# Performance work log

Hardware: AMD Instinct MI355X
Metric: run time of the kernel (lower is better)

## Reference

```python
import jax, jax.numpy as jnp
import numpy as np

# norse LIFCell defaults
DT = 1e-3
TAU_SYN_INV = 200.0   # 1 / 5e-3
TAU_MEM_INV = 100.0   # 1 / 1e-2
V_TH = 1.0
V_LEAK = 0.0
V_RESET = 0.0
ALPHA = 100.0         # superspike surrogate slope
BN_EPS = 1e-5

@jax.custom_vjp
def heaviside(x):
    return (x > 0).astype(x.dtype)

def _h_fwd(x):
    return (x > 0).astype(x.dtype), x

def _h_bwd(x, g):
    # superspike surrogate: d/dx H(x) ~ 1 / (alpha*|x| + 1)^2
    return (g / (ALPHA * jnp.abs(x) + 1.0) ** 2,)

heaviside.defvjp(_h_fwd, _h_bwd)

def _bn(x, g, b, m, v):
    # inference-mode BatchNorm1d with running stats
    return (x - m) * jax.lax.rsqrt(v + BN_EPS) * g + b

def _lif(inp, st):
    v, i = st
    v_dec = v + DT * TAU_MEM_INV * ((V_LEAK - v) + i)
    i_dec = i - DT * TAU_SYN_INV * i
    z = heaviside(v_dec - V_TH)
    v_new = (1.0 - z) * v_dec + z * V_RESET
    return z, (v_new, i_dec + inp)

B, F, T = 4096, 256, 100
H1, H2, H3, OUT = 128, 64, 32, 2

def setup_inputs():
    key = jax.random.key(0)
    ks = jax.random.split(key, 16)
    def lin(k, o, i):
        return jax.random.normal(k, (o, i), jnp.float32) / np.float32(np.sqrt(i))
    def bnp(k, n):
        k1, k2, k3, k4 = jax.random.split(k, 4)
        return (jax.random.normal(k1, (n,), jnp.float32) * 0.1 + 1.0,
                jax.random.normal(k2, (n,), jnp.float32) * 0.1,
                jax.random.normal(k3, (n,), jnp.float32) * 0.1,
                jax.random.uniform(k4, (n,), jnp.float32) + 0.5)
    bn0 = bnp(ks[0], F); bn1 = bnp(ks[1], H1); bn2 = bnp(ks[2], H2); bn3 = bnp(ks[3], H3)
    return {
        "spike_input": (jax.random.uniform(ks[4], (B, F, T)) < 0.2).astype(jnp.float32),
        "bn0_g": bn0[0], "bn0_b": bn0[1], "bn0_m": bn0[2], "bn0_v": bn0[3],
        "W1": lin(ks[5], H1, F), "b1": jnp.zeros((H1,), jnp.float32),
        "bn1_g": bn1[0], "bn1_b": bn1[1], "bn1_m": bn1[2], "bn1_v": bn1[3],
        "W2": lin(ks[6], H2, H1), "b2": jnp.zeros((H2,), jnp.float32),
        "bn2_g": bn2[0], "bn2_b": bn2[1], "bn2_m": bn2[2], "bn2_v": bn2[3],
        "W3": lin(ks[7], H3, H2), "b3": jnp.zeros((H3,), jnp.float32),
        "bn3_g": bn3[0], "bn3_b": bn3[1], "bn3_m": bn3[2], "bn3_v": bn3[3],
        "Wout": lin(ks[8], OUT, H3), "bout": jnp.zeros((OUT,), jnp.float32),
    }

def reference(spike_input, bn0_g, bn0_b, bn0_m, bn0_v,
              W1, b1, bn1_g, bn1_b, bn1_m, bn1_v,
              W2, b2, bn2_g, bn2_b, bn2_m, bn2_v,
              W3, b3, bn3_g, bn3_b, bn3_m, bn3_v,
              Wout, bout):
    bsz = spike_input.shape[0]
    dt = spike_input.dtype
    xt = jnp.transpose(spike_input, (2, 0, 1))  # [T, B, F]
    def zs(n):
        return (jnp.zeros((bsz, n), dt), jnp.zeros((bsz, n), dt))
    init = (zs(W1.shape[0]), zs(W2.shape[0]), zs(W3.shape[0]), zs(Wout.shape[0]),
            jnp.zeros((bsz, Wout.shape[0]), dt))
    def step(carry, x):
        st1, st2, st3, sto, acc = carry
        x = _bn(x, bn0_g, bn0_b, bn0_m, bn0_v)
        s1, st1 = _lif(_bn(x @ W1.T + b1, bn1_g, bn1_b, bn1_m, bn1_v), st1)
        s2, st2 = _lif(_bn(s1 @ W2.T + b2, bn2_g, bn2_b, bn2_m, bn2_v), st2)
        s3, st3 = _lif(_bn(s2 @ W3.T + b3, bn3_g, bn3_b, bn3_m, bn3_v), st3)
        so, sto = _lif(s3 @ Wout.T + bout, sto)
        return (st1, st2, st3, sto, acc + so), None
    carry, _ = jax.lax.scan(step, init, xt)
    return carry[4]  # [B, output_size] accumulated output spikes
```

## Files before the change

kernel.cpp:

```cpp
#include <hip/hip_runtime.h>
#include <stdint.h>

typedef unsigned int   uint32;
typedef unsigned short ushortT;
typedef short bf16x8 __attribute__((ext_vector_type(8)));
typedef float f32x4  __attribute__((ext_vector_type(4)));

#define T_REAL 100

#define W1S 0
#define W2S 98304
#define W3S 122880
#define WOS 129024
#define B1F 65280
#define B2F 65408
#define B3F 65472
#define BOF 65504

#define UB_BASE 33792
#define MK_BASE 68608
#define LDS_BYTES 81408

#define MFMA(a,b,c) __builtin_amdgcn_mfma_f32_16x16x32_bf16(a,b,c,0,0,0)

__device__ __forceinline__ ushortT bf16rne(float x) {
    uint32 u = __float_as_uint(x);
    return (ushortT)((u + 0x7FFFu + ((u >> 16) & 1u)) >> 16);
}

__device__ __forceinline__ void split3(float w, ushortT& a, ushortT& b, ushortT& c) {
    a = bf16rne(w); float fa = __uint_as_float((uint32)a << 16);
    float r1 = w - fa;
    b = bf16rne(r1); float fb = __uint_as_float((uint32)b << 16);
    float r2 = r1 - fb;
    c = bf16rne(r2);
}

__global__ void prep_w(const float* __restrict__ W1, const float* __restrict__ W2,
                       const float* __restrict__ W3, const float* __restrict__ Wo,
                       const float* __restrict__ bn0g, const float* __restrict__ bn0v,
                       const float* __restrict__ bn1g, const float* __restrict__ bn1v,
                       const float* __restrict__ bn2g, const float* __restrict__ bn2v,
                       const float* __restrict__ bn3g, const float* __restrict__ bn3v,
                       ushortT* __restrict__ wsS)
{
    int idx = blockIdx.x * 256 + threadIdx.x;
    float w; int base, size, off;
    if (idx < 32768) {
        int h = idx >> 8, f = idx & 255;
        float A = bn0g[f] / sqrtf(bn0v[f] + 1e-5f);
        float G = bn1g[h] / sqrtf(bn1v[h] + 1e-5f);
        w = W1[idx] * A * G; base = W1S; size = 32768; off = idx;
    } else if (idx < 40960) {
        int r = idx - 32768; int h = r >> 7;
        float G = bn2g[h] / sqrtf(bn2v[h] + 1e-5f);
        w = W2[r] * G; base = W2S; size = 8192; off = r;
    } else if (idx < 43008) {
        int r = idx - 40960; int h = r >> 6;
        float G = bn3g[h] / sqrtf(bn3v[h] + 1e-5f);
        w = W3[r] * G; base = W3S; size = 2048; off = r;
    } else if (idx < 43520) {
        int r = idx - 43008; int o = r >> 5, k = r & 31;
        w = (o < 2) ? Wo[o * 32 + k] : 0.f;
        base = WOS; size = 512; off = r;
    } else return;
    ushortT a, b, c; split3(w, a, b, c);
    wsS[base + off] = a; wsS[base + size + off] = b; wsS[base + 2 * size + off] = c;
}

__global__ void prep_bias(const float* __restrict__ bn0g, const float* __restrict__ bn0b,
                          const float* __restrict__ bn0m, const float* __restrict__ bn0v,
                          const float* __restrict__ b1,   const float* __restrict__ W1,
                          const float* __restrict__ bn1g, const float* __restrict__ bn1b,
                          const float* __restrict__ bn1m, const float* __restrict__ bn1v,
                          const float* __restrict__ b2,   const float* __restrict__ bn2g,
                          const float* __restrict__ bn2b, const float* __restrict__ bn2m,
                          const float* __restrict__ bn2v,
                          const float* __restrict__ b3,   const float* __restrict__ bn3g,
                          const float* __restrict__ bn3b, const float* __restrict__ bn3m,
                          const float* __restrict__ bn3v,
                          const float* __restrict__ bo,   float* __restrict__ wsF)
{
    __shared__ float Cs[256];
    const int tid = threadIdx.x;
    {
        float A = bn0g[tid] / sqrtf(bn0v[tid] + 1e-5f);
        Cs[tid] = bn0b[tid] - bn0m[tid] * A;
    }
    __syncthreads();
    if (tid < 128) {
        float G  = bn1g[tid] / sqrtf(bn1v[tid] + 1e-5f);
        float Bn = bn1b[tid] - bn1m[tid] * G;
        float s  = b1[tid];
        const float* wr = W1 + tid * 256;
        for (int f = 0; f < 256; ++f) s = fmaf(wr[f], Cs[f], s);
        wsF[B1F + tid] = G * s + Bn;
    }
    if (tid < 64) {
        float G = bn2g[tid] / sqrtf(bn2v[tid] + 1e-5f);
        wsF[B2F + tid] = G * b2[tid] + (bn2b[tid] - bn2m[tid] * G);
    }
    if (tid < 32) {
        float G = bn3g[tid] / sqrtf(bn3v[tid] + 1e-5f);
        wsF[B3F + tid] = G * b3[tid] + (bn3b[tid] - bn3m[tid] * G);
    }
    if (tid < 2) wsF[BOF + tid] = bo[tid];
}

__global__ __launch_bounds__(256, 2) void snn_main(
    const float* __restrict__ xin,
    const ushortT* __restrict__ wsS,
    const float* __restrict__ wsF,
    float* __restrict__ out)
{
    __shared__ uint4 ldsq[LDS_BYTES / 16];
    char* lds = (char*)ldsq;
    char* xw = lds;
    char* s1 = lds;
    char* s2 = lds;
    char* s3 = lds;
    float* u1 = (float*)(lds + UB_BASE);
    float* u2 = u1;
    float* u3 = u1;
    float* uo = u1;
    uint32* mk = (uint32*)(lds + MK_BASE);

    const int tid  = threadIdx.x;
    const int lane = tid & 63;
    const int wv   = tid >> 6;
    const int wvu  = __builtin_amdgcn_readfirstlane(wv);
    const int lr   = lane & 15;
    const int lg   = lane >> 4;
    const int b0   = blockIdx.x * 4;

    {
        const int fg = wvu;
        for (int s = 0; s < 4; ++s) {
            const float* rp = xin + ((size_t)(b0 + s) * 256 + fg * 64 + lane) * T_REAL;
            uint32* mrow = mk + (size_t)(s * 100) * 8 + fg * 2 + (lane >> 5);
#pragma unroll 1
            for (int q = 0; q < 25; ++q) {
                float4 v = *(const float4*)(rp + q * 4);
                unsigned long long bx = __ballot(v.x > 0.5f);
                unsigned long long by = __ballot(v.y > 0.5f);
                unsigned long long bz = __ballot(v.z > 0.5f);
                unsigned long long bw = __ballot(v.w > 0.5f);
                if ((lane & 31) == 0) {
                    const int sh = (lane >> 5) * 32;
                    mrow[(q * 4 + 0) * 8] = (uint32)(bx >> sh);
                    mrow[(q * 4 + 1) * 8] = (uint32)(by >> sh);
                    mrow[(q * 4 + 2) * 8] = (uint32)(bz >> sh);
                    mrow[(q * 4 + 3) * 8] = (uint32)(bw >> sh);
                }
            }
        }
    }

    float v1a = 0, i1a = 0, v1b = 0, i1b = 0;
    float v2a = 0, i2a = 0, v2b = 0, i2b = 0;
    float v3a = 0, i3a = 0, v3b = 0, i3b = 0;
    float vo = 0, io = 0, aspk = 0;

#pragma unroll 1
    for (int w = 0; w < 7; ++w) {
        const int t0 = w * 16;
        __syncthreads();

#pragma unroll
        for (int j = 0; j < 8; ++j) {
            const int c = tid + 256 * j;
            const int r = c >> 5, g = c & 31;
            const int s = r >> 4, tt = t0 + (r & 15);
            const int ttc = (tt < T_REAL) ? tt : 0;
            uint32 m = mk[(size_t)(s * 100 + ttc) * 8 + (g >> 2)];
            m = (m >> ((g & 3) * 8)) & 0xFFu;
            if (tt >= T_REAL) m = 0;
            uint32 e0 = ((m & 1u)   ? 0x3F80u : 0u) | ((m & 2u)   ? 0x3F800000u : 0u);
            uint32 e1 = ((m & 4u)   ? 0x3F80u : 0u) | ((m & 8u)   ? 0x3F800000u : 0u);
            uint32 e2 = ((m & 16u)  ? 0x3F80u : 0u) | ((m & 32u)  ? 0x3F800000u : 0u);
            uint32 e3 = ((m & 64u)  ? 0x3F80u : 0u) | ((m & 128u) ? 0x3F800000u : 0u);
            *(uint4*)(xw + (size_t)r * 528 + g * 16) = make_uint4(e0, e1, e2, e3);
        }
        __syncthreads();

        {
            const int cb = wvu * 32;
            f32x4 acc[4][2];
            const float bia0 = wsF[B1F + cb + lr];
            const float bia1 = wsF[B1F + cb + 16 + lr];
#pragma unroll
            for (int rt = 0; rt < 4; ++rt) {
                acc[rt][0] = (f32x4){bia0, bia0, bia0, bia0};
                acc[rt][1] = (f32x4){bia1, bia1, bia1, bia1};
            }
#pragma unroll
            for (int ks = 0; ks < 8; ++ks) {
                const int koff = ks * 32 + lg * 8;
                const ushortT* wb0 = wsS + W1S + (cb + lr) * 256 + koff;
                const ushortT* wb1 = wb0 + 16 * 256;
                bf16x8 B00 = *(const bf16x8*)(wb0);
                bf16x8 B01 = *(const bf16x8*)(wb0 + 32768);
                bf16x8 B02 = *(const bf16x8*)(wb0 + 65536);
                bf16x8 B10 = *(const bf16x8*)(wb1);
                bf16x8 B11 = *(const bf16x8*)(wb1 + 32768);
                bf16x8 B12 = *(const bf16x8*)(wb1 + 65536);
#pragma unroll
                for (int rt = 0; rt < 4; ++rt) {
                    bf16x8 A = *(const bf16x8*)(xw + (size_t)(rt * 16 + lr) * 528 + koff * 2);
                    acc[rt][0] = MFMA(A, B00, acc[rt][0]);
                    acc[rt][1] = MFMA(A, B10, acc[rt][1]);
                    acc[rt][0] = MFMA(A, B01, acc[rt][0]);
                    acc[rt][1] = MFMA(A, B11, acc[rt][1]);
                    acc[rt][0] = MFMA(A, B02, acc[rt][0]);
                    acc[rt][1] = MFMA(A, B12, acc[rt][1]);
                }
            }
#pragma unroll
            for (int rt = 0; rt < 4; ++rt)
#pragma unroll
                for (int ct = 0; ct < 2; ++ct) {
                    float* up = u1 + (size_t)(rt * 128 + cb + ct * 16 + lr) * 17 + lg * 4;
#pragma unroll
                    for (int j = 0; j < 4; ++j) up[j] = acc[rt][ct][j];
                }
        }
        __syncthreads();

        {
            const float* uA = u1 + (size_t)(wvu * 128 + 2 * lane) * 17;
            const float* uB = uA + 17;
            char* dst = s1 + (size_t)(wvu * 16) * 272 + lane * 4;
            float vA = v1a, iA = i1a, vB = v1b, iB = i1b;
#pragma unroll
            for (int t = 0; t < 16; ++t) {
                float vdA = vA + 0.1f * ((0.0f - vA) + iA); bool zA = vdA > 1.0f;
                vA = zA ? 0.0f : vdA; iA = (iA - 0.2f * iA) + uA[t];
                float vdB = vB + 0.1f * ((0.0f - vB) + iB); bool zB = vdB > 1.0f;
                vB = zB ? 0.0f : vdB; iB = (iB - 0.2f * iB) + uB[t];
                *(uint32*)(dst + t * 272) = (zA ? 0x3F80u : 0u) | (zB ? 0x3F800000u : 0u);
            }
            v1a = vA; i1a = iA; v1b = vB; i1b = iB;
        }
        __syncthreads();

        {
            const int cb = wvu * 16;
            f32x4 acc[4];
            const float bia = wsF[B2F + cb + lr];
#pragma unroll
            for (int rt = 0; rt < 4; ++rt) acc[rt] = (f32x4){bia, bia, bia, bia};
#pragma unroll
            for (int ks = 0; ks < 4; ++ks) {
                const int koff = ks * 32 + lg * 8;
                const ushortT* wb = wsS + W2S + (cb + lr) * 128 + koff;
                bf16x8 Bh = *(const bf16x8*)(wb);
                bf16x8 Bm = *(const bf16x8*)(wb + 8192);
                bf16x8 Bl = *(const bf16x8*)(wb + 16384);
#pragma unroll
                for (int rt = 0; rt < 4; ++rt) {
                    bf16x8 A = *(const bf16x8*)(s1 + (size_t)(rt * 16 + lr) * 272 + koff * 2);
                    acc[rt] = MFMA(A, Bh, acc[rt]);
                    acc[rt] = MFMA(A, Bm, acc[rt]);
                    acc[rt] = MFMA(A, Bl, acc[rt]);
                }
            }
#pragma unroll
            for (int rt = 0; rt < 4; ++rt) {
                float* up = u2 + (size_t)(rt * 64 + cb + lr) * 17 + lg * 4;
#pragma unroll
                for (int j = 0; j < 4; ++j) up[j] = acc[rt][j];
            }
        }
        __syncthreads();

        if (lane < 32) {
            const float* uA = u2 + (size_t)(wvu * 64 + 2 * lane) * 17;
            const float* uB = uA + 17;
            char* dst = s2 + (size_t)(wvu * 16) * 144 + lane * 4;
            float vA = v2a, iA = i2a, vB = v2b, iB = i2b;
#pragma unroll
            for (int t = 0; t < 16; ++t) {
                float vdA = vA + 0.1f * ((0.0f - vA) + iA); bool zA = vdA > 1.0f;
                vA = zA ? 0.0f : vdA; iA = (iA - 0.2f * iA) + uA[t];
                float vdB = vB + 0.1f * ((0.0f - vB) + iB); bool zB = vdB > 1.0f;
                vB = zB ? 0.0f : vdB; iB = (iB - 0.2f * iB) + uB[t];
                *(uint32*)(dst + t * 144) = (zA ? 0x3F80u : 0u) | (zB ? 0x3F800000u : 0u);
            }
            v2a = vA; i2a = iA; v2b = vB; i2b = iB;
        }
        __syncthreads();

        {
            const int rhu = wvu >> 1, chu = wvu & 1;
            const int cb = chu * 16;
            f32x4 acc[2];
            const float bia = wsF[B3F + cb + lr];
            acc[0] = (f32x4){bia, bia, bia, bia};
            acc[1] = (f32x4){bia, bia, bia, bia};
#pragma unroll
            for (int ks = 0; ks < 2; ++ks) {
                const int koff = ks * 32 + lg * 8;
                const ushortT* wb = wsS + W3S + (cb + lr) * 64 + koff;
                bf16x8 Bh = *(const bf16x8*)(wb);
                bf16x8 Bm = *(const bf16x8*)(wb + 2048);
                bf16x8 Bl = *(const bf16x8*)(wb + 4096);
#pragma unroll
                for (int r = 0; r < 2; ++r) {
                    bf16x8 A = *(const bf16x8*)(s2 + (size_t)((rhu * 2 + r) * 16 + lr) * 144 + koff * 2);
                    acc[r] = MFMA(A, Bh, acc[r]);
                    acc[r] = MFMA(A, Bm, acc[r]);
                    acc[r] = MFMA(A, Bl, acc[r]);
                }
            }
#pragma unroll
            for (int r = 0; r < 2; ++r) {
                float* up = u3 + (size_t)((rhu * 2 + r) * 32 + cb + lr) * 17 + lg * 4;
#pragma unroll
                for (int j = 0; j < 4; ++j) up[j] = acc[r][j];
            }
        }
        __syncthreads();

        if (lane < 16) {
            const float* uA = u3 + (size_t)(wvu * 32 + 2 * lane) * 17;
            const float* uB = uA + 17;
            char* dst = s3 + (size_t)(wvu * 16) * 80 + lane * 4;
            float vA = v3a, iA = i3a, vB = v3b, iB = i3b;
#pragma unroll
            for (int t = 0; t < 16; ++t) {
                float vdA = vA + 0.1f * ((0.0f - vA) + iA); bool zA = vdA > 1.0f;
                vA = zA ? 0.0f : vdA; iA = (iA - 0.2f * iA) + uA[t];
                float vdB = vB + 0.1f * ((0.0f - vB) + iB); bool zB = vdB > 1.0f;
                vB = zB ? 0.0f : vdB; iB = (iB - 0.2f * iB) + uB[t];
                *(uint32*)(dst + t * 80) = (zA ? 0x3F80u : 0u) | (zB ? 0x3F800000u : 0u);
            }
            v3a = vA; i3a = iA; v3b = vB; i3b = iB;
        }
        __syncthreads();

        {
            const float bia = (lr < 2) ? wsF[BOF + lr] : 0.f;
            f32x4 acc = (f32x4){bia, bia, bia, bia};
            const int koff = lg * 8;
            const ushortT* wb = wsS + WOS + lr * 32 + koff;
            bf16x8 Bh = *(const bf16x8*)(wb);
            bf16x8 Bm = *(const bf16x8*)(wb + 512);
            bf16x8 Bl = *(const bf16x8*)(wb + 1024);
            bf16x8 A = *(const bf16x8*)(s3 + (size_t)(wvu * 16 + lr) * 80 + koff * 2);
            acc = MFMA(A, Bh, acc);
            acc = MFMA(A, Bm, acc);
            acc = MFMA(A, Bl, acc);
            if (lr < 2) {
                float* up = uo + (size_t)(wvu * 2 + lr) * 17 + lg * 4;
#pragma unroll
                for (int j = 0; j < 4; ++j) up[j] = acc[j];
            }
        }
        __syncthreads();

        if (tid < 8) {
            const float* ur = uo + tid * 17;
            float v = vo, ii = io, a = aspk;
#pragma unroll
            for (int t = 0; t < 16; ++t) {
                float vd = v + 0.1f * ((0.0f - v) + ii);
                bool z = vd > 1.0f; v = z ? 0.0f : vd;
                ii = (ii - 0.2f * ii) + ur[t];
                if (t0 + t < T_REAL) a += z ? 1.0f : 0.0f;
            }
            vo = v; io = ii; aspk = a;
        }
    }

    if (tid < 8) out[(size_t)(b0 + (tid >> 1)) * 2 + (tid & 1)] = aspk;
}

extern "C" void kernel_launch(void* const* d_in, const int* in_sizes, int n_in,
                              void* d_out, int out_size, void* d_ws, size_t ws_size,
                              hipStream_t stream)
{
    const float* x    = (const float*)d_in[0];
    const float* bn0g = (const float*)d_in[1];
    const float* bn0b = (const float*)d_in[2];
    const float* bn0m = (const float*)d_in[3];
    const float* bn0v = (const float*)d_in[4];
    const float* W1   = (const float*)d_in[5];
    const float* b1   = (const float*)d_in[6];
    const float* bn1g = (const float*)d_in[7];
    const float* bn1b = (const float*)d_in[8];
    const float* bn1m = (const float*)d_in[9];
    const float* bn1v = (const float*)d_in[10];
    const float* W2   = (const float*)d_in[11];
    const float* b2   = (const float*)d_in[12];
    const float* bn2g = (const float*)d_in[13];
    const float* bn2b = (const float*)d_in[14];
    const float* bn2m = (const float*)d_in[15];
    const float* bn2v = (const float*)d_in[16];
    const float* W3   = (const float*)d_in[17];
    const float* b3   = (const float*)d_in[18];
    const float* bn3g = (const float*)d_in[19];
    const float* bn3b = (const float*)d_in[20];
    const float* bn3m = (const float*)d_in[21];
    const float* bn3v = (const float*)d_in[22];
    const float* Wo   = (const float*)d_in[23];
    const float* bo   = (const float*)d_in[24];

    ushortT* wsS = (ushortT*)d_ws;
    float*   wsF = (float*)d_ws;
    float*   pout = (float*)d_out;

    prep_w<<<170, 256, 0, stream>>>(W1, W2, W3, Wo, bn0g, bn0v, bn1g, bn1v,
                                    bn2g, bn2v, bn3g, bn3v, wsS);
    prep_bias<<<1, 256, 0, stream>>>(bn0g, bn0b, bn0m, bn0v, b1, W1,
                                     bn1g, bn1b, bn1m, bn1v,
                                     b2, bn2g, bn2b, bn2m, bn2v,
                                     b3, bn3g, bn3b, bn3m, bn3v, bo, wsF);
    snn_main<<<1024, 256, 0, stream>>>(x, wsS, wsF, pout);
}
```

Before: 1.036 ms.

## Store spikes as bitmasks in LDS and expand on the fly for MFMA

Replaces the dense bf16 spike tiles in LDS with packed 32-bit ballot bitmasks. Each MFMA A operand is now expanded from those masks in registers, which removes the separate input-expansion pass and its barrier. The membrane-current buffer is transposed to a time-major layout with a 260 stride, and the LIF updates become one neuron per thread using ballots. LDS use drops from about 81KB to about 31KB, so launch bounds are raised to 5 blocks per CU. The cost is extra ALU work for the expansion and an added barrier from splitting layer 1 into two halves.

```diff
diff --git a/kernel.cpp b/kernel.cpp
--- a/kernel.cpp
+++ b/kernel.cpp
@@ -17,9 +17,13 @@
 #define B3F 65472
 #define BOF 65504
 
-#define UB_BASE 33792
-#define MK_BASE 68608
-#define LDS_BYTES 81408
+#define U_B   0
+#define MK_B  16640
+#define S1_B  29440
+#define S2_B  30464
+#define S3_B  30976
+#define LDS_BYTES 31232
+#define USTR  260
 
 #define MFMA(a,b,c) __builtin_amdgcn_mfma_f32_16x16x32_bf16(a,b,c,0,0,0)
 
@@ -27,13 +31,21 @@
     uint32 u = __float_as_uint(x);
     return (ushortT)((u + 0x7FFFu + ((u >> 16) & 1u)) >> 16);
 }
-
 __device__ __forceinline__ void split3(float w, ushortT& a, ushortT& b, ushortT& c) {
     a = bf16rne(w); float fa = __uint_as_float((uint32)a << 16);
     float r1 = w - fa;
     b = bf16rne(r1); float fb = __uint_as_float((uint32)b << 16);
     float r2 = r1 - fb;
     c = bf16rne(r2);
+}
+
+__device__ __forceinline__ bf16x8 expand8(uint32 b) {
+    union { uint32 u[4]; bf16x8 v; } cv;
+    cv.u[0] = ((b & 1u)   ? 0x3F80u : 0u) | ((b & 2u)   ? 0x3F800000u : 0u);
+    cv.u[1] = ((b & 4u)   ? 0x3F80u : 0u) | ((b & 8u)   ? 0x3F800000u : 0u);
+    cv.u[2] = ((b & 16u)  ? 0x3F80u : 0u) | ((b & 32u)  ? 0x3F800000u : 0u);
+    cv.u[3] = ((b & 64u)  ? 0x3F80u : 0u) | ((b & 128u) ? 0x3F800000u : 0u);
+    return cv.v;
 }
 
 __global__ void prep_w(const float* __restrict__ W1, const float* __restrict__ W2,
@@ -107,7 +119,7 @@
     if (tid < 2) wsF[BOF + tid] = bo[tid];
 }
 
-__global__ __launch_bounds__(256, 2) void snn_main(
+__global__ __launch_bounds__(256, 5) void snn_main(
     const float* __restrict__ xin,
     const ushortT* __restrict__ wsS,
     const float* __restrict__ wsF,
@@ -115,30 +127,26 @@
 {
     __shared__ uint4 ldsq[LDS_BYTES / 16];
     char* lds = (char*)ldsq;
-    char* xw = lds;
-    char* s1 = lds;
-    char* s2 = lds;
-    char* s3 = lds;
-    float* u1 = (float*)(lds + UB_BASE);
-    float* u2 = u1;
-    float* u3 = u1;
-    float* uo = u1;
-    uint32* mk = (uint32*)(lds + MK_BASE);
+    float*  ud  = (float*)(lds + U_B);
+    uint32* mkd = (uint32*)(lds + MK_B);
+    uint32* s1d = (uint32*)(lds + S1_B);
+    uint32* s2d = (uint32*)(lds + S2_B);
+    uint32* s3d = (uint32*)(lds + S3_B);
 
     const int tid  = threadIdx.x;
     const int lane = tid & 63;
-    const int wv   = tid >> 6;
-    const int wvu  = __builtin_amdgcn_readfirstlane(wv);
+    const int wvu  = __builtin_amdgcn_readfirstlane(tid >> 6);
     const int lr   = lane & 15;
     const int lg   = lane >> 4;
     const int b0   = blockIdx.x * 4;
 
     {
         const int fg = wvu;
+        const int sh = (lane >> 5) * 32;
         for (int s = 0; s < 4; ++s) {
             const float* rp = xin + ((size_t)(b0 + s) * 256 + fg * 64 + lane) * T_REAL;
-            uint32* mrow = mk + (size_t)(s * 100) * 8 + fg * 2 + (lane >> 5);
-#pragma unroll 1
+            uint32* wr = mkd + (fg * 2 + (lane >> 5)) * 400 + s * 100;
+#pragma unroll 5
             for (int q = 0; q < 25; ++q) {
                 float4 v = *(const float4*)(rp + q * 4);
                 unsigned long long bx = __ballot(v.x > 0.5f);
@@ -146,20 +154,17 @@
                 unsigned long long bz = __ballot(v.z > 0.5f);
                 unsigned long long bw = __ballot(v.w > 0.5f);
                 if ((lane & 31) == 0) {
-                    const int sh = (lane >> 5) * 32;
-                    mrow[(q * 4 + 0) * 8] = (uint32)(bx >> sh);
-                    mrow[(q * 4 + 1) * 8] = (uint32)(by >> sh);
-                    mrow[(q * 4 + 2) * 8] = (uint32)(bz >> sh);
-                    mrow[(q * 4 + 3) * 8] = (uint32)(bw >> sh);
+                    *(uint4*)(wr + q * 4) = make_uint4((uint32)(bx >> sh), (uint32)(by >> sh),
+                                                      (uint32)(bz >> sh), (uint32)(bw >> sh));
                 }
             }
         }
     }
 
-    float v1a = 0, i1a = 0, v1b = 0, i1b = 0;
-    float v2a = 0, i2a = 0, v2b = 0, i2b = 0;
-    float v3a = 0, i3a = 0, v3b = 0, i3b = 0;
-    float vo = 0, io = 0, aspk = 0;
+    float v1h[2] = {0.f, 0.f}, i1h[2] = {0.f, 0.f};
+    float v2 = 0.f, i2 = 0.f;
+    float v3 = 0.f, i3 = 0.f;
+    float vo = 0.f, io = 0.f, aspk = 0.f;
 
 #pragma unroll 1
     for (int w = 0; w < 7; ++w) {
@@ -167,89 +172,68 @@
         __syncthreads();
 
 #pragma unroll
-        for (int j = 0; j < 8; ++j) {
-            const int c = tid + 256 * j;
-            const int r = c >> 5, g = c & 31;
-            const int s = r >> 4, tt = t0 + (r & 15);
-            const int ttc = (tt < T_REAL) ? tt : 0;
-            uint32 m = mk[(size_t)(s * 100 + ttc) * 8 + (g >> 2)];
-            m = (m >> ((g & 3) * 8)) & 0xFFu;
-            if (tt >= T_REAL) m = 0;
-            uint32 e0 = ((m & 1u)   ? 0x3F80u : 0u) | ((m & 2u)   ? 0x3F800000u : 0u);
-            uint32 e1 = ((m & 4u)   ? 0x3F80u : 0u) | ((m & 8u)   ? 0x3F800000u : 0u);
-            uint32 e2 = ((m & 16u)  ? 0x3F80u : 0u) | ((m & 32u)  ? 0x3F800000u : 0u);
-            uint32 e3 = ((m & 64u)  ? 0x3F80u : 0u) | ((m & 128u) ? 0x3F800000u : 0u);
-            *(uint4*)(xw + (size_t)r * 528 + g * 16) = make_uint4(e0, e1, e2, e3);
-        }
-        __syncthreads();
-
-        {
-            const int cb = wvu * 32;
-            f32x4 acc[4][2];
-            const float bia0 = wsF[B1F + cb + lr];
-            const float bia1 = wsF[B1F + cb + 16 + lr];
-#pragma unroll
-            for (int rt = 0; rt < 4; ++rt) {
-                acc[rt][0] = (f32x4){bia0, bia0, bia0, bia0};
-                acc[rt][1] = (f32x4){bia1, bia1, bia1, bia1};
-            }
-#pragma unroll
-            for (int ks = 0; ks < 8; ++ks) {
-                const int koff = ks * 32 + lg * 8;
-                const ushortT* wb0 = wsS + W1S + (cb + lr) * 256 + koff;
-                const ushortT* wb1 = wb0 + 16 * 256;
-                bf16x8 B00 = *(const bf16x8*)(wb0);
-                bf16x8 B01 = *(const bf16x8*)(wb0 + 32768);
-                bf16x8 B02 = *(const bf16x8*)(wb0 + 65536);
-                bf16x8 B10 = *(const bf16x8*)(wb1);
-                bf16x8 B11 = *(const bf16x8*)(wb1 + 32768);
-                bf16x8 B12 = *(const bf16x8*)(wb1 + 65536);
-#pragma unroll
-                for (int rt = 0; rt < 4; ++rt) {
-                    bf16x8 A = *(const bf16x8*)(xw + (size_t)(rt * 16 + lr) * 528 + koff * 2);
-                    acc[rt][0] = MFMA(A, B00, acc[rt][0]);
-                    acc[rt][1] = MFMA(A, B10, acc[rt][1]);
-                    acc[rt][0] = MFMA(A, B01, acc[rt][0]);
-                    acc[rt][1] = MFMA(A, B11, acc[rt][1]);
-                    acc[rt][0] = MFMA(A, B02, acc[rt][0]);
-                    acc[rt][1] = MFMA(A, B12, acc[rt][1]);
+        for (int hb = 0; hb < 2; ++hb) {
+            {
+                const int cb = wvu * 16;
+                const int hB = hb * 64 + cb;
+                const float bia = wsF[B1F + hB + lr];
+                f32x4 acc[4];
+#pragma unroll
+                for (int rt = 0; rt < 4; ++rt) acc[rt] = (f32x4){bia, bia, bia, bia};
+                const int tt = t0 + lr;
+                const int ttc = (tt < T_REAL) ? tt : (T_REAL - 1);
+#pragma unroll 2
+                for (int ks = 0; ks < 8; ++ks) {
+                    const int koff = ks * 32 + lg * 8;
+                    const ushortT* wb = wsS + W1S + (hB + lr) * 256 + koff;
+                    bf16x8 Bh = *(const bf16x8*)(wb);
+                    bf16x8 Bm = *(const bf16x8*)(wb + 32768);
+                    bf16x8 Bl = *(const bf16x8*)(wb + 65536);
+#pragma unroll
+                    for (int rt = 0; rt < 4; ++rt) {
+                        uint32 m = mkd[ks * 400 + rt * 100 + ttc];
+                        if (tt >= T_REAL) m = 0;
+                        bf16x8 A = expand8((m >> (lg * 8)) & 0xFFu);
+                        acc[rt] = MFMA(A, Bh, acc[rt]);
+                        acc[rt] = MFMA(A, Bm, acc[rt]);
+                        acc[rt] = MFMA(A, Bl, acc[rt]);
+                    }
                 }
-            }
-#pragma unroll
-            for (int rt = 0; rt < 4; ++rt)
-#pragma unroll
-                for (int ct = 0; ct < 2; ++ct) {
-                    float* up = u1 + (size_t)(rt * 128 + cb + ct * 16 + lr) * 17 + lg * 4;
-#pragma unroll
-                    for (int j = 0; j < 4; ++j) up[j] = acc[rt][ct][j];
+#pragma unroll
+                for (int rt = 0; rt < 4; ++rt)
+#pragma unroll
+                    for (int j = 0; j < 4; ++j)
+                        ud[(lg * 4 + j) * USTR + rt * 64 + cb + lr] = acc[rt][j];
+            }
+            __syncthreads();
+
+            {
+                float uu[16];
+#pragma unroll
+                for (int t = 0; t < 16; ++t) uu[t] = ud[t * USTR + tid];
+                float v = v1h[hb], ii = i1h[hb];
+#pragma unroll
+                for (int t = 0; t < 16; ++t) {
+                    float vd = v + 0.1f * ((0.0f - v) + ii);
+                    bool z = vd > 1.0f;
+                    v = z ? 0.0f : vd;
+                    ii = (ii - 0.2f * ii) + uu[t];
+                    unsigned long long bz = __ballot(z);
+                    if (lane == 0)  s1d[(hb * 2 + 0) * 64 + wvu * 16 + t] = (uint32)bz;
+                    if (lane == 32) s1d[(hb * 2 + 1) * 64 + wvu * 16 + t] = (uint32)(bz >> 32);
                 }
-        }
-        __syncthreads();
-
-        {
-            const float* uA = u1 + (size_t)(wvu * 128 + 2 * lane) * 17;
-            const float* uB = uA + 17;
-            char* dst = s1 + (size_t)(wvu * 16) * 272 + lane * 4;
-            float vA = v1a, iA = i1a, vB = v1b, iB = i1b;
-#pragma unroll
-            for (int t = 0; t < 16; ++t) {
-                float vdA = vA + 0.1f * ((0.0f - vA) + iA); bool zA = vdA > 1.0f;
-                vA = zA ? 0.0f : vdA; iA = (iA - 0.2f * iA) + uA[t];
-                float vdB = vB + 0.1f * ((0.0f - vB) + iB); bool zB = vdB > 1.0f;
-                vB = zB ? 0.0f : vdB; iB = (iB - 0.2f * iB) + uB[t];
-                *(uint32*)(dst + t * 272) = (zA ? 0x3F80u : 0u) | (zB ? 0x3F800000u : 0u);
-            }
-            v1a = vA; i1a = iA; v1b = vB; i1b = iB;
-        }
-        __syncthreads();
+                v1h[hb] = v; i1h[hb] = ii;
+            }
+            __syncthreads();
+        }
 
         {
             const int cb = wvu * 16;
+            const float bia = wsF[B2F + cb + lr];
             f32x4 acc[4];
-            const float bia = wsF[B2F + cb + lr];
 #pragma unroll
             for (int rt = 0; rt < 4; ++rt) acc[rt] = (f32x4){bia, bia, bia, bia};
-#pragma unroll
+#pragma unroll 2
             for (int ks = 0; ks < 4; ++ks) {
                 const int koff = ks * 32 + lg * 8;
                 const ushortT* wb = wsS + W2S + (cb + lr) * 128 + koff;
@@ -258,83 +242,86 @@
                 bf16x8 Bl = *(const bf16x8*)(wb + 16384);
 #pragma unroll
                 for (int rt = 0; rt < 4; ++rt) {
-                    bf16x8 A = *(const bf16x8*)(s1 + (size_t)(rt * 16 + lr) * 272 + koff * 2);
+                    uint32 m = s1d[ks * 64 + rt * 16 + lr];
+                    bf16x8 A = expand8((m >> (lg * 8)) & 0xFFu);
                     acc[rt] = MFMA(A, Bh, acc[rt]);
                     acc[rt] = MFMA(A, Bm, acc[rt]);
                     acc[rt] = MFMA(A, Bl, acc[rt]);
                 }
             }
 #pragma unroll
-            for (int rt = 0; rt < 4; ++rt) {
-                float* up = u2 + (size_t)(rt * 64 + cb + lr) * 17 + lg * 4;
-#pragma unroll
-                for (int j = 0; j < 4; ++j) up[j] = acc[rt][j];
-            }
-        }
-        __syncthreads();
-
-        if (lane < 32) {
-            const float* uA = u2 + (size_t)(wvu * 64 + 2 * lane) * 17;
-            const float* uB = uA + 17;
-            char* dst = s2 + (size_t)(wvu * 16) * 144 + lane * 4;
-            float vA = v2a, iA = i2a, vB = v2b, iB = i2b;
+            for (int rt = 0; rt < 4; ++rt)
+#pragma unroll
+                for (int j = 0; j < 4; ++j)
+                    ud[(lg * 4 + j) * USTR + rt * 64 + cb + lr] = acc[rt][j];
+        }
+        __syncthreads();
+
+        {
+            float uu[16];
+#pragma unroll
+            for (int t = 0; t < 16; ++t) uu[t] = ud[t * USTR + tid];
+            float v = v2, ii = i2;
 #pragma unroll
             for (int t = 0; t < 16; ++t) {
-                float vdA = vA + 0.1f * ((0.0f - vA) + iA); bool zA = vdA > 1.0f;
-                vA = zA ? 0.0f : vdA; iA = (iA - 0.2f * iA) + uA[t];
-                float vdB = vB + 0.1f * ((0.0f - vB) + iB); bool zB = vdB > 1.0f;
-                vB = zB ? 0.0f : vdB; iB = (iB - 0.2f * iB) + uB[t];
-                *(uint32*)(dst + t * 144) = (zA ? 0x3F80u : 0u) | (zB ? 0x3F800000u : 0u);
-            }
-            v2a = vA; i2a = iA; v2b = vB; i2b = iB;
+                float vd = v + 0.1f * ((0.0f - v) + ii);
+                bool z = vd > 1.0f;
+                v = z ? 0.0f : vd;
+                ii = (ii - 0.2f * ii) + uu[t];
+                unsigned long long bz = __ballot(z);
+                if (lane == 0)  s2d[0 * 64 + wvu * 16 + t] = (uint32)bz;
+                if (lane == 32) s2d[1 * 64 + wvu * 16 + t] = (uint32)(bz >> 32);
+            }
+            v2 = v; i2 = ii;
         }
         __syncthreads();
 
         {
             const int rhu = wvu >> 1, chu = wvu & 1;
-            const int cb = chu * 16;
+            const float bia = wsF[B3F + chu * 16 + lr];
             f32x4 acc[2];
-            const float bia = wsF[B3F + cb + lr];
             acc[0] = (f32x4){bia, bia, bia, bia};
             acc[1] = (f32x4){bia, bia, bia, bia};
 #pragma unroll
             for (int ks = 0; ks < 2; ++ks) {
                 const int koff = ks * 32 + lg * 8;
-                const ushortT* wb = wsS + W3S + (cb + lr) * 64 + koff;
+                const ushortT* wb = wsS + W3S + (chu * 16 + lr) * 64 + koff;
                 bf16x8 Bh = *(const bf16x8*)(wb);
                 bf16x8 Bm = *(const bf16x8*)(wb + 2048);
                 bf16x8 Bl = *(const bf16x8*)(wb + 4096);
 #pragma unroll
                 for (int r = 0; r < 2; ++r) {
-                    bf16x8 A = *(const bf16x8*)(s2 + (size_t)((rhu * 2 + r) * 16 + lr) * 144 + koff * 2);
+                    uint32 m = s2d[ks * 64 + (rhu * 2 + r) * 16 + lr];
+                    bf16x8 A = expand8((m >> (lg * 8)) & 0xFFu);
                     acc[r] = MFMA(A, Bh, acc[r]);
                     acc[r] = MFMA(A, Bm, acc[r]);
                     acc[r] = MFMA(A, Bl, acc[r]);
                 }
             }
 #pragma unroll
-            for (int r = 0; r < 2; ++r) {
-                float* up = u3 + (size_t)((rhu * 2 + r) * 32 + cb + lr) * 17 + lg * 4;
-#pragma unroll
-                for (int j = 0; j < 4; ++j) up[j] = acc[r][j];
-            }
-        }
-        __syncthreads();
-
-        if (lane < 16) {
-            const float* uA = u3 + (size_t)(wvu * 32 + 2 * lane) * 17;
-            const float* uB = uA + 17;
-            char* dst = s3 + (size_t)(wvu * 16) * 80 + lane * 4;
-            float vA = v3a, iA = i3a, vB = v3b, iB = i3b;
+            for (int r = 0; r < 2; ++r)
+#pragma unroll
+                for (int j = 0; j < 4; ++j)
+                    ud[(lg * 4 + j) * USTR + (rhu * 2 + r) * 32 + chu * 16 + lr] = acc[r][j];
+        }
+        __syncthreads();
+
+        if (tid < 128) {
+            float uu[16];
+#pragma unroll
+            for (int t = 0; t < 16; ++t) uu[t] = ud[t * USTR + tid];
+            float v = v3, ii = i3;
 #pragma unroll
             for (int t = 0; t < 16; ++t) {
-                float vdA = vA + 0.1f * ((0.0f - vA) + iA); bool zA = vdA > 1.0f;
-                vA = zA ? 0.0f : vdA; iA = (iA - 0.2f * iA) + uA[t];
-                float vdB = vB + 0.1f * ((0.0f - vB) + iB); bool zB = vdB > 1.0f;
-                vB = zB ? 0.0f : vdB; iB = (iB - 0.2f * iB) + uB[t];
-                *(uint32*)(dst + t * 80) = (zA ? 0x3F80u : 0u) | (zB ? 0x3F800000u : 0u);
-            }
-            v3a = vA; i3a = iA; v3b = vB; i3b = iB;
+                float vd = v + 0.1f * ((0.0f - v) + ii);
+                bool z = vd > 1.0f;
+                v = z ? 0.0f : vd;
+                ii = (ii - 0.2f * ii) + uu[t];
+                unsigned long long bz = __ballot(z);
+                if (lane == 0)  s3d[(wvu * 2 + 0) * 16 + t] = (uint32)bz;
+                if (lane == 32) s3d[(wvu * 2 + 1) * 16 + t] = (uint32)(bz >> 32);
+            }
+            v3 = v; i3 = ii;
         }
         __syncthreads();
 
@@ -346,26 +333,27 @@
             bf16x8 Bh = *(const bf16x8*)(wb);
             bf16x8 Bm = *(const bf16x8*)(wb + 512);
             bf16x8 Bl = *(const bf16x8*)(wb + 1024);
-            bf16x8 A = *(const bf16x8*)(s3 + (size_t)(wvu * 16 + lr) * 80 + koff * 2);
+            uint32 m = s3d[wvu * 16 + lr];
+            bf16x8 A = expand8((m >> (lg * 8)) & 0xFFu);
             acc = MFMA(A, Bh, acc);
             acc = MFMA(A, Bm, acc);
             acc = MFMA(A, Bl, acc);
             if (lr < 2) {
-                float* up = uo + (size_t)(wvu * 2 + lr) * 17 + lg * 4;
-#pragma unroll
-                for (int j = 0; j < 4; ++j) up[j] = acc[j];
+#pragma unroll
+                for (int j = 0; j < 4; ++j)
+                    ud[(lg * 4 + j) * USTR + wvu * 2 + lr] = acc[j];
             }
         }
         __syncthreads();
 
         if (tid < 8) {
-            const float* ur = uo + tid * 17;
             float v = vo, ii = io, a = aspk;
 #pragma unroll
             for (int t = 0; t < 16; ++t) {
                 float vd = v + 0.1f * ((0.0f - v) + ii);
-                bool z = vd > 1.0f; v = z ? 0.0f : vd;
-                ii = (ii - 0.2f * ii) + ur[t];
+                bool z = vd > 1.0f;
+                v = z ? 0.0f : vd;
+                ii = (ii - 0.2f * ii) + ud[t * USTR + tid];
                 if (t0 + t < T_REAL) a += z ? 1.0f : 0.0f;
             }
             vo = v; io = ii; aspk = a;
```

After: 1.005 ms. 1.03x faster.
